# Kernel optimization log

Measured on AMD Instinct MI355X. Metric: run time of the kernel, lower is better.

Reference implementation:

```python
import jax, jax.numpy as jnp
import numpy as np

B, T, C, H = 16, 2048, 512, 64


def _skew(x):
    # x: (B, T1, T2) -> relative-position skew trick (Music Transformer)
    b, t1, t2 = x.shape
    x = jnp.pad(x, ((0, 0), (0, 0), (1, 0)))        # pad one column on the left
    x = x.reshape(b, t2 + 1, t1)                    # reinterpret layout
    x = x[:, 1:, :]                                 # drop first row
    return jnp.transpose(x, (0, 2, 1))              # (B, T1, T2)


def setup_inputs() -> dict:
    key = jax.random.key(0)
    ks = jax.random.split(key, 5)
    return {
        "x": jax.random.normal(ks[0], (B, T, C), dtype=jnp.float32),
        "Wq": jax.random.normal(ks[1], (C, H), dtype=jnp.float32) * 0.02,
        "Wk": jax.random.normal(ks[2], (C, H), dtype=jnp.float32) * 0.02,
        "Wv": jax.random.normal(ks[3], (C, H), dtype=jnp.float32) * 0.02,
        "Er": jax.random.normal(ks[4], (T, H), dtype=jnp.float32),
    }


def reference(x, Wq, Wk, Wv, Er):
    b, t, c = x.shape
    q = x @ Wq  # (B, T, H)
    k = x @ Wk
    v = x @ Wv
    scale = 1.0 / (k.shape[-1] ** 0.5)
    att = jnp.einsum("bth,bsh->bts", q, k) * scale  # (B, T, T)
    # relative position bias via skew trick
    rel_att = jnp.einsum("bth,rh->btr", q, Er[:t])  # (B, T, T)
    att = att + _skew(rel_att)
    # causal mask
    mask = jnp.tril(jnp.ones((t, t), dtype=bool))
    att = jnp.where(mask, att, -jnp.inf)
    att = jax.nn.softmax(att, axis=-1)
    # dropout is identity in eval mode
    out = att @ v  # (B, T, H)
    return out
```

## Files before the change

### kernel.cpp

```cpp
#include <hip/hip_runtime.h>

#define NB 16
#define NT 2048
#define NC 512
#define NH 64
#define SCALE 0.125f

typedef __attribute__((ext_vector_type(8))) short bf16x8;
typedef __attribute__((ext_vector_type(16))) float f32x16;
typedef __attribute__((ext_vector_type(4))) float f32x4;
typedef __attribute__((ext_vector_type(4))) unsigned int u32x4;
typedef __attribute__((ext_vector_type(8))) unsigned short u16x8;

__device__ __forceinline__ unsigned short f2b(float f) {
    unsigned u = __builtin_bit_cast(unsigned, f);
    u = (u + 0x7fffu + ((u >> 16) & 1u)) >> 16;
    return (unsigned short)u;
}
__device__ __forceinline__ float b2f(unsigned short s) {
    return __builtin_bit_cast(float, (unsigned)s << 16);
}
#define MFMA32(a, b, c) __builtin_amdgcn_mfma_f32_32x32x16_bf16((a), (b), (c), 0, 0, 0)
#define MFMA16(a, b, c) __builtin_amdgcn_mfma_f32_16x16x32_bf16((a), (b), (c), 0, 0, 0)
#define LD8(p) (*reinterpret_cast<const bf16x8*>(p))

__global__ __launch_bounds__(256) void wcast(
    const float* __restrict__ Wq, const float* __restrict__ Wk,
    const float* __restrict__ Wv, unsigned short* __restrict__ wt)
{
    const int tid = blockIdx.x * 256 + threadIdx.x;
    const int ng = tid >> 6;
    const int k8 = tid & 63;
    const float* W = (ng < 64) ? Wq : (ng < 128 ? Wk : Wv);
    const int n = ng & 63;
    u16x8 o;
#pragma unroll
    for (int i = 0; i < 8; ++i) o[i] = f2b(W[(k8 * 8 + i) * NH + n]);
    *reinterpret_cast<u16x8*>(wt + (size_t)ng * NC + k8 * 8) = o;
}

__global__ __launch_bounds__(256) void er_cast(const float* __restrict__ er,
                                               unsigned short* __restrict__ erb)
{
    const int i = (blockIdx.x * 256 + threadIdx.x) * 4;
    float4 v = *reinterpret_cast<const float4*>(er + i);
    ushort4 o = make_ushort4(f2b(v.x), f2b(v.y), f2b(v.z), f2b(v.w));
    *reinterpret_cast<ushort4*>(erb + i) = o;
}

__global__ __launch_bounds__(64, 2) void proj_mfma(
    const float* __restrict__ x, const unsigned short* __restrict__ wt,
    unsigned short* __restrict__ qb, unsigned short* __restrict__ kb,
    unsigned short* __restrict__ vtg)
{
    const int l  = threadIdx.x;
    const int cl = l & 15;
    const int kq = l >> 4;
    const size_t t0 = (size_t)blockIdx.x * 16;

    f32x4 acc[12];
#pragma unroll
    for (int g = 0; g < 12; ++g) acc[g] = (f32x4){0.f, 0.f, 0.f, 0.f};

    const float* xr = x + (t0 + cl) * NC + kq * 8;
    const unsigned short* wrow = wt + (size_t)cl * NC + kq * 8;

    float4 xa = *reinterpret_cast<const float4*>(xr);
    float4 xb = *reinterpret_cast<const float4*>(xr + 4);

#pragma unroll
    for (int s = 0; s < 16; ++s) {
        float4 na = xa, nb = xb;
        if (s < 15) {
            na = *reinterpret_cast<const float4*>(xr + (s + 1) * 32);
            nb = *reinterpret_cast<const float4*>(xr + (s + 1) * 32 + 4);
        }
        u32x4 aw;
        aw[0] = (unsigned)f2b(xa.x) | ((unsigned)f2b(xa.y) << 16);
        aw[1] = (unsigned)f2b(xa.z) | ((unsigned)f2b(xa.w) << 16);
        aw[2] = (unsigned)f2b(xb.x) | ((unsigned)f2b(xb.y) << 16);
        aw[3] = (unsigned)f2b(xb.z) | ((unsigned)f2b(xb.w) << 16);
        const bf16x8 af = __builtin_bit_cast(bf16x8, aw);
        const unsigned short* wp = wrow + s * 32;
#pragma unroll
        for (int g = 0; g < 12; ++g)
            acc[g] = MFMA16(af, LD8(wp + (size_t)g * 16 * NC), acc[g]);
        xa = na; xb = nb;
    }

#pragma unroll
    for (int i = 0; i < 4; ++i) {
        const size_t row = t0 + kq * 4 + i;
#pragma unroll
        for (int g = 0; g < 4; ++g) {
            qb[row * NH + g * 16 + cl] = f2b(acc[g][i]);
            kb[row * NH + g * 16 + cl] = f2b(acc[g + 4][i]);
        }
    }
    const size_t bidx = t0 >> 11;
    const int tloc = (int)(t0 & 2047);
#pragma unroll
    for (int g = 0; g < 4; ++g) {
        ushort4 pv;
        pv.x = f2b(acc[g + 8][0]); pv.y = f2b(acc[g + 8][1]);
        pv.z = f2b(acc[g + 8][2]); pv.w = f2b(acc[g + 8][3]);
        *reinterpret_cast<ushort4*>(vtg + (bidx * NH + g * 16 + cl) * NT + tloc + kq * 4) = pv;
    }
}

__global__ __launch_bounds__(256, 2) void attn_mfma(
    const unsigned short* __restrict__ qb, const unsigned short* __restrict__ kb,
    const unsigned short* __restrict__ vt, const unsigned short* __restrict__ erb,
    float* __restrict__ out)
{
    __shared__ float lds[4 * 2048];

    const int tid = threadIdx.x;
    const int l  = tid & 63;
    const int w  = tid >> 6;
    const int r  = l & 31;
    const int h5 = (l >> 5) & 1;

    const int lin = blockIdx.x;
    const int bb  = lin & 15;
    const int tq  = 63 - (lin >> 4);
    const int t0  = tq * 32;

    const unsigned short* qB  = qb + (size_t)bb * NT * NH;
    const unsigned short* kB  = kb + (size_t)bb * NT * NH;
    const unsigned short* vtB = vt + (size_t)bb * NH * NT;

    float* sM = lds + w * 2048;

    const unsigned short* qp = qB + (size_t)(t0 + r) * NH + h5 * 8;
    bf16x8 qf[4];
#pragma unroll
    for (int ks = 0; ks < 4; ++ks) qf[ks] = LD8(qp + ks * 16);

    float diag = 0.f;
    {
        const unsigned short* qrow = qB + (size_t)(t0 + r) * NH;
        const unsigned short* el   = erb + (size_t)(NT - 1) * NH;
#pragma unroll
        for (int h8 = 0; h8 < 8; ++h8) {
            ushort4 qa = *reinterpret_cast<const ushort4*>(qrow + h8 * 8);
            ushort4 qc = *reinterpret_cast<const ushort4*>(qrow + h8 * 8 + 4);
            ushort4 ea = *reinterpret_cast<const ushort4*>(el + h8 * 8);
            ushort4 ec = *reinterpret_cast<const ushort4*>(el + h8 * 8 + 4);
            diag += b2f(qa.x) * b2f(ea.x) + b2f(qa.y) * b2f(ea.y)
                  + b2f(qa.z) * b2f(ea.z) + b2f(qa.w) * b2f(ea.w)
                  + b2f(qc.x) * b2f(ec.x) + b2f(qc.y) * b2f(ec.y)
                  + b2f(qc.z) * b2f(ec.z) + b2f(qc.w) * b2f(ec.w);
        }
    }

    float mrun = -1e30f, lrun = 0.f;
    f32x16 o0 = {}, o1 = {};

    const int ntiles = tq + 1;

    bf16x8 kcur[4], knxt[4];
    if (w < ntiles) {
        const unsigned short* kp = kB + (size_t)(w * 32 + r) * NH + h5 * 8;
#pragma unroll
        for (int ks = 0; ks < 4; ++ks) kcur[ks] = LD8(kp + ks * 16);
    }

    for (int it = w; it < ntiles; it += 4) {
        const int s0 = it * 32;
        const int D0 = t0 - s0;

        const int itn = it + 4;
        if (itn < ntiles) {
            const unsigned short* kp = kB + (size_t)(itn * 32 + r) * NH + h5 * 8;
#pragma unroll
            for (int ks = 0; ks < 4; ++ks) knxt[ks] = LD8(kp + ks * 16);
        }

        int arow = s0 + 1 + r; if (arow > NT - 1) arow = NT - 1;
        int e0 = D0 - 33 + r;  const int e0c = e0 < 0 ? 0 : e0;
        int e1 = e0 + 32;      const int e1c = e1 < 0 ? 0 : e1;
        const unsigned short* ap  = qB  + (size_t)arow * NH + h5 * 8;
        const unsigned short* ep0 = erb + (size_t)e0c  * NH + h5 * 8;
        const unsigned short* ep1 = erb + (size_t)e1c  * NH + h5 * 8;
        bf16x8 afr[4], ef0[4], ef1[4];
#pragma unroll
        for (int ks = 0; ks < 4; ++ks) {
            afr[ks] = LD8(ap + ks * 16);
            ef0[ks] = LD8(ep0 + ks * 16);
            ef1[ks] = LD8(ep1 + ks * 16);
        }

        f32x16 st = {};
#pragma unroll
        for (int ks = 0; ks < 4; ++ks) st = MFMA32(kcur[ks], qf[ks], st);

        f32x16 mA = {}, mB = {};
#pragma unroll
        for (int ks = 0; ks < 4; ++ks) {
            mA = MFMA32(afr[ks], ef0[ks], mA);
            mB = MFMA32(afr[ks], ef1[ks], mB);
        }

        const unsigned short* vp0 = vtB + (size_t)r        * NT + s0 + h5 * 8;
        const unsigned short* vp1 = vtB + (size_t)(r + 32) * NT + s0 + h5 * 8;
        const bf16x8 vf0a = LD8(vp0), vf0b = LD8(vp0 + 16);
        const bf16x8 vf1a = LD8(vp1), vf1b = LD8(vp1 + 16);

#pragma unroll
        for (int reg = 0; reg < 16; ++reg) {
            const int da = (reg & 3) + 8 * (reg >> 2) + 4 * h5;
            sM[da * 64 + r]      = mA[reg];
            sM[da * 64 + r + 32] = mB[reg];
        }

        float p[16];
        float mx = -1e30f;
#pragma unroll
        for (int reg = 0; reg < 16; ++reg) {
            const int dc = (reg & 3) + 8 * (reg >> 2) + 4 * h5;
            const int d  = r - dc + D0;
            float sc = st[reg] * SCALE;
            const float Mv = sM[dc * 64 + (r - dc + 31)];
            sc += (d >= 2) ? Mv : ((d == 0) ? diag : 0.0f);
            sc = (d < 0) ? -1e30f : sc;
            p[reg] = sc;
            mx = fmaxf(mx, sc);
        }
        mx = fmaxf(mx, __shfl_xor(mx, 32));
        const float mn  = fmaxf(mrun, mx);
        const float fac = __expf(mrun - mn);
        float sum = 0.f;
#pragma unroll
        for (int reg = 0; reg < 16; ++reg) {
            const float pv = __expf(p[reg] - mn);
            p[reg] = pv;
            sum += pv;
        }
        sum += __shfl_xor(sum, 32);
        lrun = lrun * fac + sum;
        mrun = mn;
        o0 *= fac;
        o1 *= fac;

        unsigned c[8];
#pragma unroll
        for (int i = 0; i < 8; ++i)
            c[i] = (unsigned)f2b(p[2 * i]) | ((unsigned)f2b(p[2 * i + 1]) << 16);
        unsigned w0, w1, w2, w3, w4, w5, w6, w7;
        {
            const unsigned s0w = (unsigned)__shfl_xor((int)c[0], 32);
            const unsigned s1w = (unsigned)__shfl_xor((int)c[1], 32);
            const unsigned s2w = (unsigned)__shfl_xor((int)c[2], 32);
            const unsigned s3w = (unsigned)__shfl_xor((int)c[3], 32);
            w0 = h5 ? s2w : c[0];   w2 = h5 ? c[2] : s0w;
            w1 = h5 ? s3w : c[1];   w3 = h5 ? c[3] : s1w;
            const unsigned s4w = (unsigned)__shfl_xor((int)c[4], 32);
            const unsigned s5w = (unsigned)__shfl_xor((int)c[5], 32);
            const unsigned s6w = (unsigned)__shfl_xor((int)c[6], 32);
            const unsigned s7w = (unsigned)__shfl_xor((int)c[7], 32);
            w4 = h5 ? s6w : c[4];   w6 = h5 ? c[6] : s4w;
            w5 = h5 ? s7w : c[5];   w7 = h5 ? c[7] : s5w;
        }
        u32x4 pa = {w0, w1, w2, w3};
        u32x4 pb = {w4, w5, w6, w7};
        const bf16x8 pf0 = __builtin_bit_cast(bf16x8, pa);
        const bf16x8 pf1 = __builtin_bit_cast(bf16x8, pb);

        o0 = MFMA32(vf0a, pf0, o0);
        o0 = MFMA32(vf0b, pf1, o0);
        o1 = MFMA32(vf1a, pf0, o1);
        o1 = MFMA32(vf1b, pf1, o1);

#pragma unroll
        for (int ks = 0; ks < 4; ++ks) kcur[ks] = knxt[ks];
    }

    __syncthreads();
    if (w > 0) {
        float* cb = lds + (size_t)(w - 1) * 2176;
        cb[l]      = mrun;
        cb[64 + l] = lrun;
#pragma unroll
        for (int e = 0; e < 16; ++e) {
            cb[128 + e * 64 + l]        = o0[e];
            cb[128 + 1024 + e * 64 + l] = o1[e];
        }
    }
    __syncthreads();
    if (w == 0) {
#pragma unroll
        for (int wv = 0; wv < 3; ++wv) {
            const float* cb = lds + (size_t)wv * 2176;
            const float mw = cb[l];
            const float lw = cb[64 + l];
            const float mn = fmaxf(mrun, mw);
            const float fa = __expf(mrun - mn);
            const float fb = __expf(mw - mn);
            lrun = lrun * fa + lw * fb;
            mrun = mn;
#pragma unroll
            for (int e = 0; e < 16; ++e) {
                o0[e] = o0[e] * fa + cb[128 + e * 64 + l] * fb;
                o1[e] = o1[e] * fa + cb[128 + 1024 + e * 64 + l] * fb;
            }
        }
        const float inv = 1.f / lrun;
        float* ob = out + (size_t)bb * NT * NH + (size_t)(t0 + r) * NH;
#pragma unroll
        for (int g = 0; g < 4; ++g) {
            float4 v0, v1;
            v0.x = o0[4 * g + 0] * inv; v0.y = o0[4 * g + 1] * inv;
            v0.z = o0[4 * g + 2] * inv; v0.w = o0[4 * g + 3] * inv;
            v1.x = o1[4 * g + 0] * inv; v1.y = o1[4 * g + 1] * inv;
            v1.z = o1[4 * g + 2] * inv; v1.w = o1[4 * g + 3] * inv;
            *reinterpret_cast<float4*>(ob + 8 * g + 4 * h5)      = v0;
            *reinterpret_cast<float4*>(ob + 32 + 8 * g + 4 * h5) = v1;
        }
    }
}

extern "C" void kernel_launch(void* const* d_in, const int* in_sizes, int n_in,
                              void* d_out, int out_size, void* d_ws, size_t ws_size,
                              hipStream_t stream) {
    (void)in_sizes; (void)n_in; (void)out_size; (void)ws_size;
    const float* x  = (const float*)d_in[0];
    const float* Wq = (const float*)d_in[1];
    const float* Wk = (const float*)d_in[2];
    const float* Wv = (const float*)d_in[3];
    const float* Er = (const float*)d_in[4];
    float* outp = (float*)d_out;

    const size_t BTH = (size_t)NB * NT * NH;
    unsigned short* qbp = (unsigned short*)d_ws;
    unsigned short* kbp = qbp + BTH;
    unsigned short* vtp = kbp + BTH;
    unsigned short* erp = vtp + BTH;
    unsigned short* wtp = erp + (size_t)NT * NH;

    wcast  <<<dim3(48),  dim3(256), 0, stream>>>(Wq, Wk, Wv, wtp);
    er_cast<<<dim3(128), dim3(256), 0, stream>>>(Er, erp);
    proj_mfma<<<dim3(NB * NT / 16), dim3(64), 0, stream>>>(x, wtp, qbp, kbp, vtp);
    attn_mfma<<<dim3(NB * (NT / 32)), dim3(256), 0, stream>>>(qbp, kbp, vtp, erp, outp);
}
```

Measured before the change: 248.5 us.

## Stage projection weights in LDS via async loads, packed bf16 converts, MFMA priority

The projection kernel now uses 256-thread blocks covering 64 rows. Weights are pre-laid-out in MFMA fragment order and double-buffered into shared memory with global_load_lds, so each weight tile is read once per block instead of once per 16-row wave. Scalar bf16 rounding is replaced with the hardware packed convert instruction in several places, and the attention kernel raises wave priority around its MFMA sections. This adds a barrier and vmcnt wait per k-step in the projection. The hardware convert may round differently from the software rounding.

Result: faster. 207.2 us (-16.6%).

```diff
diff --git a/kernel.cpp b/kernel.cpp
--- a/kernel.cpp
+++ b/kernel.cpp
@@ -20,23 +20,32 @@
 __device__ __forceinline__ float b2f(unsigned short s) {
     return __builtin_bit_cast(float, (unsigned)s << 16);
 }
+__device__ __forceinline__ unsigned cvt_pk_bf16(float lo, float hi) {
+    unsigned r;
+    asm("v_cvt_pk_bf16_f32 %0, %1, %2" : "=v"(r) : "v"(lo), "v"(hi));
+    return r;
+}
 #define MFMA32(a, b, c) __builtin_amdgcn_mfma_f32_32x32x16_bf16((a), (b), (c), 0, 0, 0)
 #define MFMA16(a, b, c) __builtin_amdgcn_mfma_f32_16x16x32_bf16((a), (b), (c), 0, 0, 0)
 #define LD8(p) (*reinterpret_cast<const bf16x8*>(p))
 
 __global__ __launch_bounds__(256) void wcast(
     const float* __restrict__ Wq, const float* __restrict__ Wk,
-    const float* __restrict__ Wv, unsigned short* __restrict__ wt)
+    const float* __restrict__ Wv, unsigned short* __restrict__ wfrag)
 {
-    const int tid = blockIdx.x * 256 + threadIdx.x;
-    const int ng = tid >> 6;
-    const int k8 = tid & 63;
-    const float* W = (ng < 64) ? Wq : (ng < 128 ? Wk : Wv);
-    const int n = ng & 63;
+    const int idx = blockIdx.x * 256 + threadIdx.x;
+    const int kstep = idx / 768;
+    const int rem   = idx % 768;
+    const int g = rem >> 6;
+    const int l = rem & 63;
+    const int n  = g * 16 + (l & 15);
+    const int kb = kstep * 32 + ((l >> 4) << 3);
+    const float* W = (n < 64) ? Wq : (n < 128 ? Wk : Wv);
+    const int col = n & 63;
     u16x8 o;
 #pragma unroll
-    for (int i = 0; i < 8; ++i) o[i] = f2b(W[(k8 * 8 + i) * NH + n]);
-    *reinterpret_cast<u16x8*>(wt + (size_t)ng * NC + k8 * 8) = o;
+    for (int j = 0; j < 8; ++j) o[j] = f2b(W[(size_t)(kb + j) * NH + col]);
+    *reinterpret_cast<u16x8*>(wfrag + (size_t)idx * 8) = o;
 }
 
 __global__ __launch_bounds__(256) void er_cast(const float* __restrict__ er,
@@ -48,63 +57,86 @@
     *reinterpret_cast<ushort4*>(erb + i) = o;
 }
 
-__global__ __launch_bounds__(64, 2) void proj_mfma(
-    const float* __restrict__ x, const unsigned short* __restrict__ wt,
+__global__ __launch_bounds__(256, 2) void proj_mfma(
+    const float* __restrict__ x, const unsigned short* __restrict__ wfrag,
     unsigned short* __restrict__ qb, unsigned short* __restrict__ kb,
     unsigned short* __restrict__ vtg)
 {
-    const int l  = threadIdx.x;
+    __shared__ unsigned short wsh[2][6144];
+
+    const int tid = threadIdx.x;
+    const int w = tid >> 6;
+    const int l = tid & 63;
     const int cl = l & 15;
     const int kq = l >> 4;
-    const size_t t0 = (size_t)blockIdx.x * 16;
+
+    const size_t t0w = (size_t)blockIdx.x * 64 + w * 16;
+    const float* xr = x + (t0w + cl) * NC + kq * 8;
 
     f32x4 acc[12];
 #pragma unroll
     for (int g = 0; g < 12; ++g) acc[g] = (f32x4){0.f, 0.f, 0.f, 0.f};
 
-    const float* xr = x + (t0 + cl) * NC + kq * 8;
-    const unsigned short* wrow = wt + (size_t)cl * NC + kq * 8;
-
+#pragma unroll
+    for (int j = 0; j < 3; ++j) {
+        const int c = w * 3 + j;
+        const unsigned short* gsrc = wfrag + ((size_t)(0 * 12 + c) * 64 + l) * 8;
+        __builtin_amdgcn_global_load_lds(
+            (const __attribute__((address_space(1))) void*)gsrc,
+            (__attribute__((address_space(3))) void*)&wsh[0][c * 512], 16, 0, 0);
+    }
     float4 xa = *reinterpret_cast<const float4*>(xr);
     float4 xb = *reinterpret_cast<const float4*>(xr + 4);
 
-#pragma unroll
-    for (int s = 0; s < 16; ++s) {
+    for (int k = 0; k < 16; ++k) {
+        const int buf = k & 1;
+        asm volatile("s_waitcnt vmcnt(0)" ::: "memory");
+        __syncthreads();
         float4 na = xa, nb = xb;
-        if (s < 15) {
-            na = *reinterpret_cast<const float4*>(xr + (s + 1) * 32);
-            nb = *reinterpret_cast<const float4*>(xr + (s + 1) * 32 + 4);
+        if (k < 15) {
+#pragma unroll
+            for (int j = 0; j < 3; ++j) {
+                const int c = w * 3 + j;
+                const unsigned short* gsrc = wfrag + ((size_t)((k + 1) * 12 + c) * 64 + l) * 8;
+                __builtin_amdgcn_global_load_lds(
+                    (const __attribute__((address_space(1))) void*)gsrc,
+                    (__attribute__((address_space(3))) void*)&wsh[buf ^ 1][c * 512], 16, 0, 0);
+            }
+            na = *reinterpret_cast<const float4*>(xr + (k + 1) * 32);
+            nb = *reinterpret_cast<const float4*>(xr + (k + 1) * 32 + 4);
         }
         u32x4 aw;
-        aw[0] = (unsigned)f2b(xa.x) | ((unsigned)f2b(xa.y) << 16);
-        aw[1] = (unsigned)f2b(xa.z) | ((unsigned)f2b(xa.w) << 16);
-        aw[2] = (unsigned)f2b(xb.x) | ((unsigned)f2b(xb.y) << 16);
-        aw[3] = (unsigned)f2b(xb.z) | ((unsigned)f2b(xb.w) << 16);
+        aw[0] = cvt_pk_bf16(xa.x, xa.y);
+        aw[1] = cvt_pk_bf16(xa.z, xa.w);
+        aw[2] = cvt_pk_bf16(xb.x, xb.y);
+        aw[3] = cvt_pk_bf16(xb.z, xb.w);
         const bf16x8 af = __builtin_bit_cast(bf16x8, aw);
-        const unsigned short* wp = wrow + s * 32;
-#pragma unroll
-        for (int g = 0; g < 12; ++g)
-            acc[g] = MFMA16(af, LD8(wp + (size_t)g * 16 * NC), acc[g]);
+#pragma unroll
+        for (int g = 0; g < 12; ++g) {
+            const bf16x8 bf = *reinterpret_cast<const bf16x8*>(&wsh[buf][g * 512 + l * 8]);
+            acc[g] = MFMA16(af, bf, acc[g]);
+        }
         xa = na; xb = nb;
     }
 
 #pragma unroll
     for (int i = 0; i < 4; ++i) {
-        const size_t row = t0 + kq * 4 + i;
+        const size_t row = t0w + kq * 4 + i;
 #pragma unroll
         for (int g = 0; g < 4; ++g) {
             qb[row * NH + g * 16 + cl] = f2b(acc[g][i]);
             kb[row * NH + g * 16 + cl] = f2b(acc[g + 4][i]);
         }
     }
-    const size_t bidx = t0 >> 11;
-    const int tloc = (int)(t0 & 2047);
+    const size_t rowb = t0w + kq * 4;
+    const size_t bidx = rowb >> 11;
+    const int tloc = (int)(rowb & 2047);
 #pragma unroll
     for (int g = 0; g < 4; ++g) {
-        ushort4 pv;
-        pv.x = f2b(acc[g + 8][0]); pv.y = f2b(acc[g + 8][1]);
-        pv.z = f2b(acc[g + 8][2]); pv.w = f2b(acc[g + 8][3]);
-        *reinterpret_cast<ushort4*>(vtg + (bidx * NH + g * 16 + cl) * NT + tloc + kq * 4) = pv;
+        unsigned u0 = cvt_pk_bf16(acc[g + 8][0], acc[g + 8][1]);
+        unsigned u1 = cvt_pk_bf16(acc[g + 8][2], acc[g + 8][3]);
+        uint2 pv = make_uint2(u0, u1);
+        *reinterpret_cast<uint2*>(vtg + (bidx * NH + g * 16 + cl) * NT + tloc) = pv;
     }
 }
 
@@ -191,16 +223,17 @@
             ef1[ks] = LD8(ep1 + ks * 16);
         }
 
+        __builtin_amdgcn_s_setprio(1);
         f32x16 st = {};
 #pragma unroll
         for (int ks = 0; ks < 4; ++ks) st = MFMA32(kcur[ks], qf[ks], st);
-
         f32x16 mA = {}, mB = {};
 #pragma unroll
         for (int ks = 0; ks < 4; ++ks) {
             mA = MFMA32(afr[ks], ef0[ks], mA);
             mB = MFMA32(afr[ks], ef1[ks], mB);
         }
+        __builtin_amdgcn_s_setprio(0);
 
         const unsigned short* vp0 = vtB + (size_t)r        * NT + s0 + h5 * 8;
         const unsigned short* vp1 = vtB + (size_t)(r + 32) * NT + s0 + h5 * 8;
@@ -246,7 +279,7 @@
         unsigned c[8];
 #pragma unroll
         for (int i = 0; i < 8; ++i)
-            c[i] = (unsigned)f2b(p[2 * i]) | ((unsigned)f2b(p[2 * i + 1]) << 16);
+            c[i] = cvt_pk_bf16(p[2 * i], p[2 * i + 1]);
         unsigned w0, w1, w2, w3, w4, w5, w6, w7;
         {
             const unsigned s0w = (unsigned)__shfl_xor((int)c[0], 32);
@@ -267,10 +300,12 @@
         const bf16x8 pf0 = __builtin_bit_cast(bf16x8, pa);
         const bf16x8 pf1 = __builtin_bit_cast(bf16x8, pb);
 
+        __builtin_amdgcn_s_setprio(1);
         o0 = MFMA32(vf0a, pf0, o0);
         o0 = MFMA32(vf0b, pf1, o0);
         o1 = MFMA32(vf1a, pf0, o1);
         o1 = MFMA32(vf1b, pf1, o1);
+        __builtin_amdgcn_s_setprio(0);
 
 #pragma unroll
         for (int ks = 0; ks < 4; ++ks) kcur[ks] = knxt[ks];
@@ -336,10 +371,10 @@
     unsigned short* kbp = qbp + BTH;
     unsigned short* vtp = kbp + BTH;
     unsigned short* erp = vtp + BTH;
-    unsigned short* wtp = erp + (size_t)NT * NH;
-
-    wcast  <<<dim3(48),  dim3(256), 0, stream>>>(Wq, Wk, Wv, wtp);
+    unsigned short* wfp = erp + (size_t)NT * NH;
+
+    wcast  <<<dim3(48),  dim3(256), 0, stream>>>(Wq, Wk, Wv, wfp);
     er_cast<<<dim3(128), dim3(256), 0, stream>>>(Er, erp);
-    proj_mfma<<<dim3(NB * NT / 16), dim3(64), 0, stream>>>(x, wtp, qbp, kbp, vtp);
+    proj_mfma<<<dim3(NB * NT / 64), dim3(256), 0, stream>>>(x, wfp, qbp, kbp, vtp);
     attn_mfma<<<dim3(NB * (NT / 32)), dim3(256), 0, stream>>>(qbp, kbp, vtp, erp, outp);
 }
```
